# Optimization experiments

Measured on AMD Instinct MI355X. Metric: run time of the kernel, lower is better.

Reference implementation:

```python
import jax, jax.numpy as jnp
import numpy as np

BASELINE_THRE = 0.1
BETA = 1.8  # is_adapt=True
R_M = 3.0
DT = 1.0

IN_DIM = 2048
R_IN = 2048
R_OUT = 2048
HIDDEN = R_IN + R_OUT
BATCH = 1024


def _xavier(key, fan_out, fan_in):
    bound = jnp.sqrt(6.0 / (fan_in + fan_out)).astype(jnp.float32)
    return jax.random.uniform(key, (fan_out, fan_in), jnp.float32, -bound, bound)


def _linear_bias(key, fan_out, fan_in):
    # torch nn.Linear default bias init: U(-1/sqrt(fan_in), 1/sqrt(fan_in))
    bound = 1.0 / np.sqrt(fan_in)
    return jax.random.uniform(key, (fan_out,), jnp.float32, -bound, bound)


def setup_inputs() -> dict:
    key = jax.random.key(0)
    ks = jax.random.split(key, 16)
    return {
        "x_t": jax.random.normal(ks[0], (BATCH, IN_DIM), jnp.float32),
        "mem_t": jax.random.normal(ks[1], (BATCH, HIDDEN), jnp.float32),
        "spk_t": (jax.random.uniform(ks[2], (BATCH, HIDDEN)) < 0.3).astype(jnp.float32),
        "b_t": jax.random.uniform(ks[3], (BATCH, HIDDEN), jnp.float32),
        "W_x2in": _xavier(ks[4], R_IN, IN_DIM),
        "b_x2in": _linear_bias(ks[5], R_IN, IN_DIM),
        "W_rec4in": _xavier(ks[6], R_IN, R_IN),
        "b_rec4in": _linear_bias(ks[7], R_IN, R_IN),
        "W_in2out": _xavier(ks[8], R_OUT, R_IN),
        "b_in2out": _linear_bias(ks[9], R_OUT, R_IN),
        "W_rec4out": _xavier(ks[10], R_OUT, R_OUT),
        "b_rec4out": _linear_bias(ks[11], R_OUT, R_OUT),
        "W_out2in": _xavier(ks[12], R_IN, R_OUT),
        "b_out2in": _linear_bias(ks[13], R_IN, R_OUT),
        "tau_adp": 4.6 + 0.1 * jax.random.normal(ks[14], (HIDDEN,), jnp.float32),
        "tau_m": 3.0 + 0.1 * jax.random.normal(ks[15], (HIDDEN,), jnp.float32),
    }


# surrogate spike: heaviside fwd, gaussian surrogate grad (gamma=0.5, lens=0.5)
GAMMA = 0.5
LENS = 0.5

@jax.custom_vjp
def spike_fn(x):
    return (x > 0).astype(x.dtype)

def _spike_fwd(x):
    return spike_fn(x), x

def _spike_bwd(x, g):
    sur = GAMMA * jnp.exp(-(x * x) / (2.0 * LENS * LENS)) / (np.sqrt(2.0 * np.pi) * LENS)
    return (g * sur,)

spike_fn.defvjp(_spike_fwd, _spike_bwd)


def reference(x_t, mem_t, spk_t, b_t,
              W_x2in, b_x2in, W_rec4in, b_rec4in, W_in2out, b_in2out,
              W_rec4out, b_rec4out, W_out2in, b_out2in, tau_adp, tau_m):
    spk_out = spk_t[:, :R_OUT]   # first r_out neurons are the "out" population
    spk_in = spk_t[:, R_OUT:]    # remaining r_in neurons

    x = x_t @ W_x2in.T + b_x2in
    r_in_ = x + (spk_in @ W_rec4in.T + b_rec4in) + (spk_out @ W_out2in.T + b_out2in)
    r_out_ = (spk_out @ W_rec4out.T + b_rec4out) + (spk_in @ W_in2out.T + b_in2out)
    inputs = jnp.concatenate((r_out_, r_in_), axis=1)  # [B, HIDDEN]

    tau_m_s = jax.nn.sigmoid(tau_m)
    tau_adp_s = jax.nn.sigmoid(tau_adp)

    b = tau_adp_s * b_t + (1.0 - tau_adp_s) * spk_t
    new_thre = BASELINE_THRE + BETA * b
    mem = mem_t * tau_m_s + (1.0 - tau_m_s) * R_M * inputs - new_thre * spk_t * DT
    spike = spike_fn(mem - new_thre)
    return (mem, spike, b)
```

## Files before the change

kernel.cpp:

```cpp
#include <hip/hip_runtime.h>

#define HID   4096
#define NHALF 2048
#define BKS   16
#define WS_SLICE 2097152
#define WS_BYTES_NEEDED (5L * WS_SLICE * 4L)

typedef unsigned short u16;
typedef __attribute__((ext_vector_type(8))) unsigned short ushort8;
typedef __attribute__((ext_vector_type(4))) unsigned short ushort4_t;

__device__ __forceinline__ float sigf(float x) { return 1.0f / (1.0f + expf(-x)); }
__device__ __forceinline__ float bf2f(u16 u) { return __uint_as_float(((unsigned)u) << 16); }


__launch_bounds__(64, 2)
__global__ void snn_seg_kernel(
    const void* __restrict__ x_t, const void* __restrict__ spk_t,
    const void* __restrict__ W_x2in, const void* __restrict__ W_rec4in,
    const void* __restrict__ W_in2out, const void* __restrict__ W_rec4out,
    const void* __restrict__ W_out2in, float* __restrict__ ws)
{
    __shared__ float As[BKS * 128];
    __shared__ float Bs[BKS * 64];

    const int t = threadIdx.x;

    bool cond = false;
    if (t < 32) {
        const u16* xu = (const u16*)x_t;
        const float v = fabsf(bf2f(xu[2 * t]));
        cond = (v >= 0.0009765625f && v <= 16.0f);
    }
    const bool B2 = __popcll(__ballot(cond)) >= 28;

    const int b = blockIdx.x;
    const int hlf = (b >= 512) ? 1 : 0;
    const int r = hlf ? (b - 512) : b;
    const int seg = r >> 8;
    const int tile = r & 255;
    const int m0 = (tile >> 5) * 128;
    const int n0 = (tile & 31) * 64;

    const void* ab; long astr; const void* bb; int slot;
    const long spkoff = (B2 ? 2L : 4L) * NHALF;
    if (!hlf) {
        slot = seg;
        if (seg == 0) { ab = spk_t; astr = HID; bb = W_rec4out; }
        else { ab = (const void*)((const char*)spk_t + spkoff); astr = HID; bb = W_in2out; }
    } else {
        slot = 2 + seg;
        if (seg == 0) { ab = x_t; astr = 2048; bb = W_x2in; }
        else if (seg == 1) { ab = (const void*)((const char*)spk_t + spkoff); astr = HID; bb = W_rec4in; }
        else { ab = spk_t; astr = HID; bb = W_out2in; }
    }

    const int tr = t >> 3;
    const int tc = t & 7;

    auto load16 = [&](const void* base, long eoff, float* d) {
        if (B2) {
            const u16* p = (const u16*)base + eoff;
            const ushort8 v0 = *(const ushort8*)p;
            const ushort8 v1 = *(const ushort8*)(p + 8);
#pragma unroll
            for (int e = 0; e < 8; ++e) { d[e] = bf2f(v0[e]); d[8 + e] = bf2f(v1[e]); }
        } else {
            const float* p = (const float*)base + eoff;
            const float4 x0 = *(const float4*)(p);
            const float4 x1 = *(const float4*)(p + 4);
            const float4 x2 = *(const float4*)(p + 8);
            const float4 x3 = *(const float4*)(p + 12);
            d[0]  = x0.x; d[1]  = x0.y; d[2]  = x0.z; d[3]  = x0.w;
            d[4]  = x1.x; d[5]  = x1.y; d[6]  = x1.z; d[7]  = x1.w;
            d[8]  = x2.x; d[9]  = x2.y; d[10] = x2.z; d[11] = x2.w;
            d[12] = x3.x; d[13] = x3.y; d[14] = x3.z; d[15] = x3.w;
        }
    };

    float acc[16][8];
#pragma unroll
    for (int i = 0; i < 16; ++i)
#pragma unroll
        for (int j = 0; j < 8; ++j) acc[i][j] = 0.0f;

    const long arow0 = (long)(m0 + t) * astr;
    const long arow1 = (long)(m0 + 64 + t) * astr;
    const long brow  = (long)(n0 + t) * 2048;
    float av0[16], av1[16], bv[16];
    load16(ab, arow0, av0);
    load16(ab, arow1, av1);
    load16(bb, brow, bv);

    for (int s = 0; s < 2048 / BKS; ++s) {
        __syncthreads();
#pragma unroll
        for (int e = 0; e < BKS; ++e) {
            As[e * 128 + t]      = av0[e];
            As[e * 128 + 64 + t] = av1[e];
            Bs[e * 64 + t]       = bv[e];
        }
        __syncthreads();
        if (s + 1 < 2048 / BKS) {
            const long k0 = (long)(s + 1) * BKS;
            load16(ab, arow0 + k0, av0);
            load16(ab, arow1 + k0, av1);
            load16(bb, brow + k0, bv);
        }
#pragma unroll 4
        for (int k = 0; k < BKS; ++k) {
            const float* ak = &As[k * 128];
            const float* bk = &Bs[k * 64];
            const float4 A0 = *(const float4*)(ak + tr * 4);
            const float4 A1 = *(const float4*)(ak + 32 + tr * 4);
            const float4 A2 = *(const float4*)(ak + 64 + tr * 4);
            const float4 A3 = *(const float4*)(ak + 96 + tr * 4);
            const float4 B0 = *(const float4*)(bk + tc * 4);
            const float4 B1 = *(const float4*)(bk + 32 + tc * 4);
            const float a[16] = {A0.x, A0.y, A0.z, A0.w, A1.x, A1.y, A1.z, A1.w,
                                 A2.x, A2.y, A2.z, A2.w, A3.x, A3.y, A3.z, A3.w};
            const float c[8]  = {B0.x, B0.y, B0.z, B0.w, B1.x, B1.y, B1.z, B1.w};
#pragma unroll
            for (int i = 0; i < 16; ++i)
#pragma unroll
                for (int j = 0; j < 8; ++j)
                    acc[i][j] = fmaf(a[i], c[j], acc[i][j]);
        }
    }

    float* wbase = ws + (long)slot * WS_SLICE;
#pragma unroll
    for (int i = 0; i < 16; ++i) {
        const int m = m0 + tr * 4 + (i & 3) + (i >> 2) * 32;
#pragma unroll
        for (int jq = 0; jq < 2; ++jq) {
            const long off = (long)m * 2048 + n0 + jq * 32 + tc * 4;
            *(float4*)(wbase + off) = make_float4(acc[i][jq * 4 + 0], acc[i][jq * 4 + 1],
                                                  acc[i][jq * 4 + 2], acc[i][jq * 4 + 3]);
        }
    }
}

__launch_bounds__(256)
__global__ void snn_epi_kernel(
    const void* __restrict__ mem_t, const void* __restrict__ spk_t, const void* __restrict__ b_t,
    const void* __restrict__ b_x2in, const void* __restrict__ b_rec4in,
    const void* __restrict__ b_in2out, const void* __restrict__ b_rec4out,
    const void* __restrict__ b_out2in,
    const void* __restrict__ tau_adp, const void* __restrict__ tau_m,
    const float* __restrict__ ws, float* __restrict__ out)
{
    __shared__ int s_flags;
    const int t = threadIdx.x;

    bool c2l = false, c1l = false;
    if (t < 32) {
        const u16* mu = (const u16*)mem_t;
        const float v = fabsf(bf2f(mu[2 * t]));
        c2l = (v >= 0.0009765625f && v <= 16.0f);
    } else if (t < 64) {
        const u16* tu = (const u16*)tau_adp;
        const float w = bf2f(tu[2 * (t - 32)]);
        c1l = (w >= 3.5f && w <= 6.0f);
    }
    const unsigned long long bal2 = __ballot(c2l);
    const unsigned long long bal1 = __ballot(c1l);
    if (t == 0)
        s_flags = ((__popcll(bal2 & 0xffffffffull) >= 28) ? 1 : 0) |
                  ((__popcll(bal1 >> 32) >= 28) ? 2 : 0);
    __syncthreads();
    const bool B2 = (s_flags & 1) != 0;
    const bool B1 = (s_flags & 2) != 0;

    auto g1d = [&](const void* p, long i) -> float {
        return B1 ? bf2f(((const u16*)p)[i]) : ((const float*)p)[i];
    };
    auto load4g = [&](const void* base, long eoff, float* d) {
        if (B2) {
            const ushort4_t v = *(const ushort4_t*)((const u16*)base + eoff);
#pragma unroll
            for (int e = 0; e < 4; ++e) d[e] = bf2f(v[e]);
        } else {
            const float4 v = *(const float4*)((const float*)base + eoff);
            d[0] = v.x; d[1] = v.y; d[2] = v.z; d[3] = v.w;
        }
    };

    const long idx = ((long)blockIdx.x * 256 + t) * 4;
    const int m = (int)(idx >> 12);
    const int c = (int)(idx & 4095);
    const int hlf = c >> 11;

    const long poff = (long)m * 2048 + (c & 2047);
    float inp[4];
    if (!hlf) {
        const float4 p0 = *(const float4*)(ws + poff);
        const float4 p1 = *(const float4*)(ws + WS_SLICE + poff);
        inp[0] = p0.x + p1.x; inp[1] = p0.y + p1.y; inp[2] = p0.z + p1.z; inp[3] = p0.w + p1.w;
    } else {
        const float4 p2 = *(const float4*)(ws + 2L * WS_SLICE + poff);
        const float4 p3 = *(const float4*)(ws + 3L * WS_SLICE + poff);
        const float4 p4 = *(const float4*)(ws + 4L * WS_SLICE + poff);
        inp[0] = p2.x + p3.x + p4.x; inp[1] = p2.y + p3.y + p4.y;
        inp[2] = p2.z + p3.z + p4.z; inp[3] = p2.w + p3.w + p4.w;
    }

    const long base = (long)m * HID + c;
    float sp[4], bt[4], mt[4];
    load4g(spk_t, base, sp);
    load4g(b_t,   base, bt);
    load4g(mem_t, base, mt);

    float om[4], os[4], ob[4];
#pragma unroll
    for (int j = 0; j < 4; ++j) {
        const int n = (c & 2047) + j;
        const int jg = c + j;
        const float bias = hlf
            ? g1d(b_x2in, n) + g1d(b_rec4in, n) + g1d(b_out2in, n)
            : g1d(b_rec4out, n) + g1d(b_in2out, n);
        const float tm = sigf(g1d(tau_m, jg));
        const float ta = sigf(g1d(tau_adp, jg));
        const float in2 = inp[j] + bias;
        const float bb = ta * bt[j] + (1.0f - ta) * sp[j];
        const float thre = 0.1f + 1.8f * bb;
        const float mem = mt[j] * tm + (1.0f - tm) * 3.0f * in2 - thre * sp[j];
        om[j] = mem;
        os[j] = (mem - thre) > 0.0f ? 1.0f : 0.0f;
        ob[j] = bb;
    }
    *(float4*)(out + base)           = make_float4(om[0], om[1], om[2], om[3]);
    *(float4*)(out + 4194304 + base) = make_float4(os[0], os[1], os[2], os[3]);
    *(float4*)(out + 8388608 + base) = make_float4(ob[0], ob[1], ob[2], ob[3]);
}

__launch_bounds__(256, 2)
__global__ void snn_fused_kernel(
    const void* __restrict__ x_t,
    const void* __restrict__ mem_t,
    const void* __restrict__ spk_t,
    const void* __restrict__ b_t,
    const void* __restrict__ W_x2in,    const void* __restrict__ b_x2in,
    const void* __restrict__ W_rec4in,  const void* __restrict__ b_rec4in,
    const void* __restrict__ W_in2out,  const void* __restrict__ b_in2out,
    const void* __restrict__ W_rec4out, const void* __restrict__ b_rec4out,
    const void* __restrict__ W_out2in,  const void* __restrict__ b_out2in,
    const void* __restrict__ tau_adp,   const void* __restrict__ tau_m,
    float*      __restrict__ out)
{
    __shared__ float As[32 * 132];
    __shared__ float Bs[32 * 68];
    __shared__ int s_flags;

    const int t = threadIdx.x;
    if (t == 0) {
        const u16* xu = (const u16*)x_t;
        const u16* tu = (const u16*)tau_adp;
        int c2 = 0, c1 = 0;
        for (int i = 0; i < 32; ++i) {
            float v = fabsf(bf2f(xu[2 * i]));
            if (v >= 0.0009765625f && v <= 16.0f) ++c2;
            float w = bf2f(tu[2 * i]);
            if (w >= 3.5f && w <= 6.0f) ++c1;
        }
        s_flags = ((c2 >= 28) ? 1 : 0) | ((c1 >= 28) ? 2 : 0);
    }
    __syncthreads();
    const bool B2 = (s_flags & 1) != 0;
    const bool B1 = (s_flags & 2) != 0;

    const int m0  = blockIdx.x * 128;
    const int hlf = blockIdx.y >> 5;
    const int n0  = (blockIdx.y & 31) * 64;

    const int tr = t >> 4;
    const int tc = t & 15;
    const int sm = t >> 1;
    const int sj = (t & 1) * 16;
    const int smB = t & 63;
    const int sjB = (t >> 6) * 8;

    auto load16 = [&](const void* base, long eoff, float* d) {
        if (B2) {
            const u16* p = (const u16*)base + eoff;
            const ushort8 v0 = *(const ushort8*)p;
            const ushort8 v1 = *(const ushort8*)(p + 8);
#pragma unroll
            for (int e = 0; e < 8; ++e) { d[e] = bf2f(v0[e]); d[8 + e] = bf2f(v1[e]); }
        } else {
            const float* p = (const float*)base + eoff;
            const float4 x0 = *(const float4*)(p);
            const float4 x1 = *(const float4*)(p + 4);
            const float4 x2 = *(const float4*)(p + 8);
            const float4 x3 = *(const float4*)(p + 12);
            d[0] = x0.x; d[1] = x0.y; d[2] = x0.z; d[3] = x0.w;
            d[4] = x1.x; d[5] = x1.y; d[6] = x1.z; d[7] = x1.w;
            d[8] = x2.x; d[9] = x2.y; d[10] = x2.z; d[11] = x2.w;
            d[12] = x3.x; d[13] = x3.y; d[14] = x3.z; d[15] = x3.w;
        }
    };
    auto load8 = [&](const void* base, long eoff, float* d) {
        if (B2) {
            const ushort8 v0 = *(const ushort8*)((const u16*)base + eoff);
#pragma unroll
            for (int e = 0; e < 8; ++e) d[e] = bf2f(v0[e]);
        } else {
            const float* p = (const float*)base + eoff;
            const float4 x0 = *(const float4*)(p);
            const float4 x1 = *(const float4*)(p + 4);
            d[0] = x0.x; d[1] = x0.y; d[2] = x0.z; d[3] = x0.w;
            d[4] = x1.x; d[5] = x1.y; d[6] = x1.z; d[7] = x1.w;
        }
    };
    auto load4g = [&](const void* base, long eoff, float* d) {
        if (B2) {
            const ushort4_t v = *(const ushort4_t*)((const u16*)base + eoff);
#pragma unroll
            for (int e = 0; e < 4; ++e) d[e] = bf2f(v[e]);
        } else {
            const float4 v = *(const float4*)((const float*)base + eoff);
            d[0] = v.x; d[1] = v.y; d[2] = v.z; d[3] = v.w;
        }
    };
    auto g1d = [&](const void* base, long i) -> float {
        return B1 ? bf2f(((const u16*)base)[i]) : ((const float*)base)[i];
    };

    float acc[8][4];
#pragma unroll
    for (int i = 0; i < 8; ++i)
#pragma unroll
        for (int j = 0; j < 4; ++j) acc[i][j] = 0.0f;

    auto seg = [&](const void* abase, int astr, const void* bbase) {
        float av[16], bv[8];
        load16(abase, (long)(m0 + sm) * astr + sj, av);
        load8(bbase, (long)(n0 + smB) * 2048 + sjB, bv);
        for (int s = 0; s < 64; ++s) {
            __syncthreads();
#pragma unroll
            for (int e = 0; e < 16; ++e) As[(sj + e) * 132 + sm] = av[e];
#pragma unroll
            for (int e = 0; e < 8; ++e)  Bs[(sjB + e) * 68 + smB] = bv[e];
            __syncthreads();
            if (s + 1 < 64) {
                load16(abase, (long)(m0 + sm) * astr + (s + 1) * 32 + sj, av);
                load8(bbase, (long)(n0 + smB) * 2048 + (s + 1) * 32 + sjB, bv);
            }
#pragma unroll 4
            for (int k = 0; k < 32; ++k) {
                const float* ak = &As[k * 132];
                const float* bk = &Bs[k * 68];
                const float4 A0 = *(const float4*)(ak + tr * 4);
                const float4 A1 = *(const float4*)(ak + 64 + tr * 4);
                const float4 B0 = *(const float4*)(bk + tc * 4);
                const float a[8] = {A0.x, A0.y, A0.z, A0.w, A1.x, A1.y, A1.z, A1.w};
                const float b[4] = {B0.x, B0.y, B0.z, B0.w};
#pragma unroll
                for (int i = 0; i < 8; ++i)
#pragma unroll
                    for (int j = 0; j < 4; ++j)
                        acc[i][j] = fmaf(a[i], b[j], acc[i][j]);
            }
        }
    };

    const long spk_half_off = (B2 ? 2L : 4L) * NHALF;
    if (hlf == 0) {
        seg(spk_t, HID, W_rec4out);
        seg((const void*)((const char*)spk_t + spk_half_off), HID, W_in2out);
    } else {
        seg(x_t, 2048, W_x2in);
        seg((const void*)((const char*)spk_t + spk_half_off), HID, W_rec4in);
        seg(spk_t, HID, W_out2in);
    }

    const int jbase = hlf * NHALF;
    float biasj[4], tmj[4], taj[4];
#pragma unroll
    for (int j = 0; j < 4; ++j) {
        const int n  = n0 + tc * 4 + j;
        const int jg = jbase + n;
        biasj[j] = (hlf == 0)
            ? g1d(b_rec4out, n) + g1d(b_in2out, n)
            : g1d(b_x2in, n) + g1d(b_rec4in, n) + g1d(b_out2in, n);
        tmj[j] = sigf(g1d(tau_m, jg));
        taj[j] = sigf(g1d(tau_adp, jg));
    }
#pragma unroll
    for (int i = 0; i < 8; ++i) {
        const int m = m0 + tr * 4 + (i & 3) + ((i >> 2) * 64);
        const long base = (long)m * HID + jbase + n0 + tc * 4;
        float sp[4], bt[4], mt[4];
        load4g(spk_t, base, sp);
        load4g(b_t,   base, bt);
        load4g(mem_t, base, mt);
        float om[4], os[4], ob[4];
#pragma unroll
        for (int j = 0; j < 4; ++j) {
            const float inp  = acc[i][j] + biasj[j];
            const float bb   = taj[j] * bt[j] + (1.0f - taj[j]) * sp[j];
            const float thre = 0.1f + 1.8f * bb;
            const float mem  = mt[j] * tmj[j] + (1.0f - tmj[j]) * 3.0f * inp - thre * sp[j];
            om[j] = mem;
            os[j] = (mem - thre) > 0.0f ? 1.0f : 0.0f;
            ob[j] = bb;
        }
        *(float4*)(out + base)           = make_float4(om[0], om[1], om[2], om[3]);
        *(float4*)(out + 4194304 + base) = make_float4(os[0], os[1], os[2], os[3]);
        *(float4*)(out + 8388608 + base) = make_float4(ob[0], ob[1], ob[2], ob[3]);
    }
}

__global__ void shape_marker_kernel(float* __restrict__ out, float val) {
    if (threadIdx.x == 0 && blockIdx.x == 0) out[0] = val;
}

extern "C" void kernel_launch(void* const* d_in, const int* in_sizes, int n_in,
                              void* d_out, int out_size, void* d_ws, size_t ws_size,
                              hipStream_t stream) {
    float* out = (float*)d_out;

    if (d_ws != nullptr && ws_size >= (size_t)WS_BYTES_NEEDED) {
        snn_seg_kernel<<<1280, 64, 0, stream>>>(
            d_in[0], d_in[2], d_in[4], d_in[6], d_in[8], d_in[10], d_in[12],
            (float*)d_ws);
        snn_epi_kernel<<<4096, 256, 0, stream>>>(
            d_in[1], d_in[2], d_in[3], d_in[5], d_in[7], d_in[9], d_in[11],
            d_in[13], d_in[14], d_in[15], (const float*)d_ws, out);
    } else {
        snn_fused_kernel<<<dim3(8, 64), dim3(256), 0, stream>>>(
            d_in[0], d_in[1], d_in[2], d_in[3],
            d_in[4], d_in[5], d_in[6], d_in[7], d_in[8], d_in[9],
            d_in[10], d_in[11], d_in[12], d_in[13], d_in[14], d_in[15], out);
    }

    static const int expect[16] = {
        2097152, 4194304, 4194304, 4194304,
        4194304, 2048, 4194304, 2048, 4194304, 2048,
        4194304, 2048, 4194304, 2048, 4096, 4096};
    int bad = -1;
    if (n_in != 16) bad = 17;
    else {
        for (int i = 0; i < 16; ++i)
            if (in_sizes[i] != expect[i]) { bad = i; break; }
        if (bad < 0 && out_size != 12582912) bad = 16;
    }
    if (bad >= 0)
        shape_marker_kernel<<<1, 64, 0, stream>>>(out, 50000.0f + 512.0f * bad);
}
```

Baseline: 813.8 us.

## Split GEMM segments along K and stage partials in output planes

Each segment GEMM is split into two K halves, so the grid doubles to 2560 single-wavefront blocks. The aim is better CU occupancy and load balance on the many-CU device. Ten partial products are now written: some go into the three output planes as scratch and the rest into workspace slices, which lowers the workspace requirement. The epilogue sums four or six partials instead of two or three. This adds epilogue read traffic and relies on each thread reading its output locations before overwriting them.

```diff
diff --git a/kernel.cpp b/kernel.cpp
--- a/kernel.cpp
+++ b/kernel.cpp
@@ -3,8 +3,9 @@
 #define HID   4096
 #define NHALF 2048
 #define BKS   16
+#define OPLANE 4194304
 #define WS_SLICE 2097152
-#define WS_BYTES_NEEDED (5L * WS_SLICE * 4L)
+#define WS_BYTES_NEEDED (4L * WS_SLICE * 4L)
 
 typedef unsigned short u16;
 typedef __attribute__((ext_vector_type(8))) unsigned short ushort8;
@@ -19,7 +20,8 @@
     const void* __restrict__ x_t, const void* __restrict__ spk_t,
     const void* __restrict__ W_x2in, const void* __restrict__ W_rec4in,
     const void* __restrict__ W_in2out, const void* __restrict__ W_rec4out,
-    const void* __restrict__ W_out2in, float* __restrict__ ws)
+    const void* __restrict__ W_out2in, float* __restrict__ ws,
+    float* __restrict__ out)
 {
     __shared__ float As[BKS * 128];
     __shared__ float Bs[BKS * 64];
@@ -35,42 +37,48 @@
     const bool B2 = __popcll(__ballot(cond)) >= 28;
 
     const int b = blockIdx.x;
-    const int hlf = (b >= 512) ? 1 : 0;
-    const int r = hlf ? (b - 512) : b;
-    const int seg = r >> 8;
-    const int tile = r & 255;
+    const int kh = (b >= 1280) ? 1 : 0;
+    const int r0 = b - kh * 1280;
+    const int hlf = (r0 >= 512) ? 1 : 0;
+    const int rr = hlf ? (r0 - 512) : r0;
+    const int seg = rr >> 8;
+    const int tile = rr & 255;
     const int m0 = (tile >> 5) * 128;
     const int n0 = (tile & 31) * 64;
-
-    const void* ab; long astr; const void* bb; int slot;
+    const long koff = (long)kh * 1024;
+
+    const void* ab; long astr; const void* bb;
     const long spkoff = (B2 ? 2L : 4L) * NHALF;
     if (!hlf) {
-        slot = seg;
         if (seg == 0) { ab = spk_t; astr = HID; bb = W_rec4out; }
         else { ab = (const void*)((const char*)spk_t + spkoff); astr = HID; bb = W_in2out; }
     } else {
-        slot = 2 + seg;
         if (seg == 0) { ab = x_t; astr = 2048; bb = W_x2in; }
         else if (seg == 1) { ab = (const void*)((const char*)spk_t + spkoff); astr = HID; bb = W_rec4in; }
         else { ab = spk_t; astr = HID; bb = W_out2in; }
     }
 
+    const int p = kh * (hlf ? 3 : 2) + seg;
+    float* dst; long ldst;
+    if (p < 3) { dst = out + (long)p * OPLANE + (hlf ? 2048 : 0); ldst = 4096; }
+    else       { dst = ws + (long)(hlf ? (p - 3) : 3) * WS_SLICE; ldst = 2048; }
+
     const int tr = t >> 3;
     const int tc = t & 7;
 
     auto load16 = [&](const void* base, long eoff, float* d) {
         if (B2) {
-            const u16* p = (const u16*)base + eoff;
-            const ushort8 v0 = *(const ushort8*)p;
-            const ushort8 v1 = *(const ushort8*)(p + 8);
+            const u16* pp = (const u16*)base + eoff;
+            const ushort8 v0 = *(const ushort8*)pp;
+            const ushort8 v1 = *(const ushort8*)(pp + 8);
 #pragma unroll
             for (int e = 0; e < 8; ++e) { d[e] = bf2f(v0[e]); d[8 + e] = bf2f(v1[e]); }
         } else {
-            const float* p = (const float*)base + eoff;
-            const float4 x0 = *(const float4*)(p);
-            const float4 x1 = *(const float4*)(p + 4);
-            const float4 x2 = *(const float4*)(p + 8);
-            const float4 x3 = *(const float4*)(p + 12);
+            const float* pp = (const float*)base + eoff;
+            const float4 x0 = *(const float4*)(pp);
+            const float4 x1 = *(const float4*)(pp + 4);
+            const float4 x2 = *(const float4*)(pp + 8);
+            const float4 x3 = *(const float4*)(pp + 12);
             d[0]  = x0.x; d[1]  = x0.y; d[2]  = x0.z; d[3]  = x0.w;
             d[4]  = x1.x; d[5]  = x1.y; d[6]  = x1.z; d[7]  = x1.w;
             d[8]  = x2.x; d[9]  = x2.y; d[10] = x2.z; d[11] = x2.w;
@@ -84,15 +92,15 @@
 #pragma unroll
         for (int j = 0; j < 8; ++j) acc[i][j] = 0.0f;
 
-    const long arow0 = (long)(m0 + t) * astr;
-    const long arow1 = (long)(m0 + 64 + t) * astr;
-    const long brow  = (long)(n0 + t) * 2048;
+    const long arow0 = (long)(m0 + t) * astr + koff;
+    const long arow1 = (long)(m0 + 64 + t) * astr + koff;
+    const long brow  = (long)(n0 + t) * 2048 + koff;
     float av0[16], av1[16], bv[16];
     load16(ab, arow0, av0);
     load16(ab, arow1, av1);
     load16(bb, brow, bv);
 
-    for (int s = 0; s < 2048 / BKS; ++s) {
+    for (int s = 0; s < 1024 / BKS; ++s) {
         __syncthreads();
 #pragma unroll
         for (int e = 0; e < BKS; ++e) {
@@ -101,7 +109,7 @@
             Bs[e * 64 + t]       = bv[e];
         }
         __syncthreads();
-        if (s + 1 < 2048 / BKS) {
+        if (s + 1 < 1024 / BKS) {
             const long k0 = (long)(s + 1) * BKS;
             load16(ab, arow0 + k0, av0);
             load16(ab, arow1 + k0, av1);
@@ -128,15 +136,14 @@
         }
     }
 
-    float* wbase = ws + (long)slot * WS_SLICE;
 #pragma unroll
     for (int i = 0; i < 16; ++i) {
         const int m = m0 + tr * 4 + (i & 3) + (i >> 2) * 32;
 #pragma unroll
         for (int jq = 0; jq < 2; ++jq) {
-            const long off = (long)m * 2048 + n0 + jq * 32 + tc * 4;
-            *(float4*)(wbase + off) = make_float4(acc[i][jq * 4 + 0], acc[i][jq * 4 + 1],
-                                                  acc[i][jq * 4 + 2], acc[i][jq * 4 + 3]);
+            const long off = (long)m * ldst + n0 + jq * 32 + tc * 4;
+            *(float4*)(dst + off) = make_float4(acc[i][jq * 4 + 0], acc[i][jq * 4 + 1],
+                                                acc[i][jq * 4 + 2], acc[i][jq * 4 + 3]);
         }
     }
 }
@@ -191,21 +198,32 @@
     const int c = (int)(idx & 4095);
     const int hlf = c >> 11;
 
-    const long poff = (long)m * 2048 + (c & 2047);
+    const long base = (long)m * HID + c;
+    const long woff = (long)m * 2048 + (c & 2047);
+
     float inp[4];
-    if (!hlf) {
-        const float4 p0 = *(const float4*)(ws + poff);
-        const float4 p1 = *(const float4*)(ws + WS_SLICE + poff);
-        inp[0] = p0.x + p1.x; inp[1] = p0.y + p1.y; inp[2] = p0.z + p1.z; inp[3] = p0.w + p1.w;
-    } else {
-        const float4 p2 = *(const float4*)(ws + 2L * WS_SLICE + poff);
-        const float4 p3 = *(const float4*)(ws + 3L * WS_SLICE + poff);
-        const float4 p4 = *(const float4*)(ws + 4L * WS_SLICE + poff);
-        inp[0] = p2.x + p3.x + p4.x; inp[1] = p2.y + p3.y + p4.y;
-        inp[2] = p2.z + p3.z + p4.z; inp[3] = p2.w + p3.w + p4.w;
-    }
-
-    const long base = (long)m * HID + c;
+    {
+        const float4 q0 = *(const float4*)(out + base);
+        const float4 q1 = *(const float4*)(out + OPLANE + base);
+        if (!hlf) {
+            const float4 q2 = *(const float4*)(out + 2L * OPLANE + base);
+            const float4 w3 = *(const float4*)(ws + 3L * WS_SLICE + woff);
+            inp[0] = q0.x + q1.x + q2.x + w3.x;
+            inp[1] = q0.y + q1.y + q2.y + w3.y;
+            inp[2] = q0.z + q1.z + q2.z + w3.z;
+            inp[3] = q0.w + q1.w + q2.w + w3.w;
+        } else {
+            const float4 q2 = *(const float4*)(out + 2L * OPLANE + base);
+            const float4 w0 = *(const float4*)(ws + woff);
+            const float4 w1 = *(const float4*)(ws + WS_SLICE + woff);
+            const float4 w2 = *(const float4*)(ws + 2L * WS_SLICE + woff);
+            inp[0] = q0.x + q1.x + q2.x + w0.x + w1.x + w2.x;
+            inp[1] = q0.y + q1.y + q2.y + w0.y + w1.y + w2.y;
+            inp[2] = q0.z + q1.z + q2.z + w0.z + w1.z + w2.z;
+            inp[3] = q0.w + q1.w + q2.w + w0.w + w1.w + w2.w;
+        }
+    }
+
     float sp[4], bt[4], mt[4];
     load4g(spk_t, base, sp);
     load4g(b_t,   base, bt);
@@ -229,9 +247,9 @@
         os[j] = (mem - thre) > 0.0f ? 1.0f : 0.0f;
         ob[j] = bb;
     }
-    *(float4*)(out + base)           = make_float4(om[0], om[1], om[2], om[3]);
-    *(float4*)(out + 4194304 + base) = make_float4(os[0], os[1], os[2], os[3]);
-    *(float4*)(out + 8388608 + base) = make_float4(ob[0], ob[1], ob[2], ob[3]);
+    *(float4*)(out + base)              = make_float4(om[0], om[1], om[2], om[3]);
+    *(float4*)(out + OPLANE + base)     = make_float4(os[0], os[1], os[2], os[3]);
+    *(float4*)(out + 2L * OPLANE + base) = make_float4(ob[0], ob[1], ob[2], ob[3]);
 }
 
 __launch_bounds__(256, 2)
@@ -422,9 +440,9 @@
     float* out = (float*)d_out;
 
     if (d_ws != nullptr && ws_size >= (size_t)WS_BYTES_NEEDED) {
-        snn_seg_kernel<<<1280, 64, 0, stream>>>(
+        snn_seg_kernel<<<2560, 64, 0, stream>>>(
             d_in[0], d_in[2], d_in[4], d_in[6], d_in[8], d_in[10], d_in[12],
-            (float*)d_ws);
+            (float*)d_ws, out);
         snn_epi_kernel<<<4096, 256, 0, stream>>>(
             d_in[1], d_in[2], d_in[3], d_in[5], d_in[7], d_in[9], d_in[11],
             d_in[13], d_in[14], d_in[15], (const float*)d_ws, out);
```

Result: faster. 702.1 us (-13.7%).
